# Optimization experiments

Measured on AMD Instinct MI355X. Metric: run time of the kernel, lower is better.

The kernel has to match this reference:

```python
import jax, jax.numpy as jnp
import numpy as np

G_K = 16
BN_EPS = 1e-5


def knn_idx(x, k):
    # x: (B, N, C) -> idx: (B, N, k) indices of k nearest neighbors (incl. self)
    sq = jnp.sum(x * x, axis=-1)                       # (B, N)
    d = sq[:, :, None] + sq[:, None, :] - 2.0 * jnp.einsum('bnc,bmc->bnm', x, x)
    _, idx = jax.lax.top_k(-d, k)                      # smallest distances
    return idx


def setup_inputs() -> dict:
    key = jax.random.key(0)
    k1, k2 = jax.random.split(key)
    B, N, C, D = 4, 8192, 3, 64
    x = jax.random.normal(k1, (B, N, C), dtype=jnp.float32)
    W = jax.random.normal(k2, (3 * C, D), dtype=jnp.float32) * 0.1
    b = jnp.zeros((D,), dtype=jnp.float32)
    gamma = jnp.ones((D,), dtype=jnp.float32)
    beta = jnp.zeros((D,), dtype=jnp.float32)
    return {"x": x, "W": W, "b": b, "gamma": gamma, "beta": beta}


def reference(x, W, b, gamma, beta):
    # KNN query (int indices, non-differentiable as in torch)
    idx = knn_idx(x, G_K)                              # (B, N, k)
    # gather-group neighbors: (B, N, k, C)
    x_ne = jax.vmap(lambda xb, ib: xb[ib])(x, idx)
    x_ce = jnp.broadcast_to(x[:, :, None, :], x_ne.shape)
    feat = jnp.concatenate([x_ce, x_ne - x_ce, x_ne], axis=-1)  # (B, N, k, 3C)
    # 1x1 conv == per-(point,neighbor) linear
    h = jnp.einsum('bnkc,cd->bnkd', feat, W) + b       # (B, N, k, D)
    # BatchNorm over (B, N, k) per channel (training-mode batch stats)
    mean = jnp.mean(h, axis=(0, 1, 2))
    var = jnp.var(h, axis=(0, 1, 2))
    h = gamma * (h - mean) * jax.lax.rsqrt(var + BN_EPS) + beta
    h = jax.nn.relu(h)
    # max-pool over neighbors k
    return jnp.max(h, axis=2)                          # (B, N, D)
```

## Files before the change

kernel.cpp:

```cpp
#include <hip/hip_runtime.h>

#define NPTS 8192
#define NB 4
#define KNN 16
#define DCH 64
#define CAP 128
#define WR 8

#define WS_XQ 0
#define WS_IB 524288
#define WS_ST 1572864
#define WS_SS 1573376

__device__ __forceinline__ float distf(float4 a, float4 c) {
    float dot = __fmaf_rn(a.x, c.x, __fmaf_rn(a.y, c.y, a.z * c.z));
    return __fmaf_rn(-2.0f, dot, a.w + c.w);
}

__global__ __launch_bounds__(256) void k1_prep(const float* __restrict__ x, float4* __restrict__ xq) {
    int p = blockIdx.x * 256 + threadIdx.x;
    if (p >= NB * NPTS) return;
    float x0 = x[p * 3 + 0], x1 = x[p * 3 + 1], x2 = x[p * 3 + 2];
    float sq = __fmaf_rn(x0, x0, __fmaf_rn(x1, x1, x2 * x2));
    xq[p] = make_float4(x0, x1, x2, sq);
}

__global__ __launch_bounds__(256, 4) void k2_knn(const float4* __restrict__ xq,
                                                 unsigned short* __restrict__ ibuf) {
    __shared__ float2 buf[4][WR][CAP];
    __shared__ float vmin[4][WR][64];
    const int wave = threadIdx.x >> 6;
    const int lane = threadIdx.x & 63;
    const int b = blockIdx.x >> 8;
    const int blkrow = (blockIdx.x & 255) * (4 * WR);
    const float4* xb = xq + b * NPTS;
    const int rowbase = blkrow + wave * WR;

    float4 xi[WR];
#pragma unroll
    for (int r = 0; r < WR; ++r) xi[r] = xb[rowbase + r];

    float mn[WR];
#pragma unroll
    for (int r = 0; r < WR; ++r) mn[r] = 3.0e38f;

#pragma unroll 2
    for (int c0 = 0; c0 < NPTS; c0 += 64) {
        float4 cj = xb[c0 + lane];
#pragma unroll
        for (int r = 0; r < WR; ++r) mn[r] = fminf(mn[r], distf(xi[r], cj));
    }

#pragma unroll
    for (int r = 0; r < WR; ++r) vmin[wave][r][lane] = mn[r];
    __syncthreads();

    float tau[WR];
#pragma unroll
    for (int r = 0; r < WR; ++r) {
        float mine = mn[r];
        int rk = 0;
        const float4* vm4 = (const float4*)(&vmin[wave][r][0]);
#pragma unroll
        for (int q = 0; q < 16; ++q) {
            float4 vv = vm4[q];
            int j0 = q * 4;
            rk += (vv.x < mine || (vv.x == mine && (j0 + 0) < lane)) ? 1 : 0;
            rk += (vv.y < mine || (vv.y == mine && (j0 + 1) < lane)) ? 1 : 0;
            rk += (vv.z < mine || (vv.z == mine && (j0 + 2) < lane)) ? 1 : 0;
            rk += (vv.w < mine || (vv.w == mine && (j0 + 3) < lane)) ? 1 : 0;
        }
        float v = (rk < KNN) ? mine : -3.0e38f;
#pragma unroll
        for (int o = 32; o > 0; o >>= 1) v = fmaxf(v, __shfl_xor(v, o));
        tau[r] = v;
    }

    int cnt[WR];
#pragma unroll
    for (int r = 0; r < WR; ++r) cnt[r] = 0;

#pragma unroll 2
    for (int c0 = 0; c0 < NPTS; c0 += 64) {
        float4 cj = xb[c0 + lane];
        float fidx = (float)(c0 + lane);
#pragma unroll
        for (int r = 0; r < WR; ++r) {
            float d = distf(xi[r], cj);
            bool pass = (d <= tau[r]);
            unsigned long long m = __ballot(pass);
            if (m) {
                if (pass) {
                    int ofs = __builtin_amdgcn_mbcnt_hi((unsigned)(m >> 32),
                              __builtin_amdgcn_mbcnt_lo((unsigned)m, 0));
                    int pos = cnt[r] + ofs;
                    if (pos < CAP) buf[wave][r][pos] = make_float2(d, fidx);
                }
                cnt[r] += (int)__popcll(m);
            }
        }
    }

    __syncthreads();

#pragma unroll
    for (int rr = 0; rr < WR; ++rr) {
        int n = cnt[rr];
        n = (n < CAP) ? n : CAP;
        int l1 = lane + 64;
        bool v0 = (lane < n), v1 = (l1 < n);
        float2 e0 = buf[wave][rr][v0 ? lane : 0];
        float2 e1 = buf[wave][rr][v1 ? l1 : 0];
        int r0 = 0, r1 = 0;
        for (int j = 0; j < n; ++j) {
            float2 fj = buf[wave][rr][j];
            r0 += (fj.x < e0.x || (fj.x == e0.x && fj.y < e0.y)) ? 1 : 0;
            r1 += (fj.x < e1.x || (fj.x == e1.x && fj.y < e1.y)) ? 1 : 0;
        }
        size_t grow = (size_t)(b * NPTS + rowbase + rr) * KNN;
        if (v0 && r0 < KNN) ibuf[grow + r0] = (unsigned short)(int)e0.y;
        if (v1 && r1 < KNN) ibuf[grow + r1] = (unsigned short)(int)e1.y;
    }
}

__global__ __launch_bounds__(256) void k3_moments(const float4* __restrict__ xq,
                                                  const unsigned short* __restrict__ ibuf,
                                                  double* __restrict__ stats) {
    __shared__ float red[4][54];
    int p = blockIdx.x * 256 + threadIdx.x;
    int b = p >> 13;
    const float4* xb = xq + b * NPTS;
    const unsigned short* ib = ibuf + (size_t)p * KNN;
    float4 xi = xb[p & (NPTS - 1)];

    float acc[54];
#pragma unroll
    for (int i = 0; i < 54; ++i) acc[i] = 0.0f;

#pragma unroll
    for (int k = 0; k < KNN; ++k) {
        int j = ib[k];
        float4 cj = xb[j];
        float f[9] = {xi.x, xi.y, xi.z, cj.x - xi.x, cj.y - xi.y, cj.z - xi.z, cj.x, cj.y, cj.z};
        int t = 9;
#pragma unroll
        for (int a = 0; a < 9; ++a) {
            acc[a] += f[a];
#pragma unroll
            for (int c = a; c < 9; ++c) { acc[t] += f[a] * f[c]; ++t; }
        }
    }

#pragma unroll
    for (int i = 0; i < 54; ++i) {
        float v = acc[i];
        for (int o = 32; o > 0; o >>= 1) v += __shfl_down(v, o);
        acc[i] = v;
    }
    int lane = threadIdx.x & 63;
    int wv = threadIdx.x >> 6;
    if (lane == 0) {
#pragma unroll
        for (int i = 0; i < 54; ++i) red[wv][i] = acc[i];
    }
    __syncthreads();
    if (threadIdx.x < 54) {
        float s = red[0][threadIdx.x] + red[1][threadIdx.x] + red[2][threadIdx.x] + red[3][threadIdx.x];
        atomicAdd(&stats[threadIdx.x], (double)s);
    }
}

__global__ void k4_finalize(const double* __restrict__ stats, const float* __restrict__ W,
                            const float* __restrict__ bias, const float* __restrict__ gamma,
                            const float* __restrict__ beta, float* __restrict__ ss) {
    int d = threadIdx.x;
    if (d >= DCH) return;
    const double M = (double)NB * NPTS * KNN;
    double w[9];
    for (int c = 0; c < 9; ++c) w[c] = (double)W[c * DCH + d];
    double mf[9];
    for (int a = 0; a < 9; ++a) mf[a] = stats[a] / M;
    double q1 = 0.0;
    for (int a = 0; a < 9; ++a) q1 += mf[a] * w[a];
    double q2 = 0.0;
    int t = 0;
    for (int a = 0; a < 9; ++a) {
        for (int c = a; c < 9; ++c) {
            double pv = stats[9 + t] / M;
            double term = pv * w[a] * w[c];
            q2 += (a == c) ? term : 2.0 * term;
            ++t;
        }
    }
    double bd = (double)bias[d];
    double mean = q1 + bd;
    double ehh = q2 + 2.0 * bd * q1 + bd * bd;
    double var = ehh - mean * mean;
    double sc = (double)gamma[d] / sqrt(var + 1e-5);
    double sh = (double)beta[d] + sc * (bd - mean);
    ss[d] = (float)sc;
    ss[DCH + d] = (float)sh;
}

__global__ __launch_bounds__(256) void k5_out(const float4* __restrict__ xq,
                                              const unsigned short* __restrict__ ibuf,
                                              const float* __restrict__ W, const float* __restrict__ ss,
                                              float* __restrict__ out) {
    __shared__ float Ws[9 * DCH];
    __shared__ float scs[DCH], shs[DCH];
    for (int i = threadIdx.x; i < 9 * DCH; i += 256) Ws[i] = W[i];
    if (threadIdx.x < DCH) {
        scs[threadIdx.x] = ss[threadIdx.x];
        shs[threadIdx.x] = ss[DCH + threadIdx.x];
    }
    __syncthreads();

    int pt = blockIdx.x * 32 + (threadIdx.x >> 3);
    int oc = (threadIdx.x & 7) * 8;
    int b = pt >> 13;
    const float4* xb = xq + b * NPTS;
    float4 xi = xb[pt & (NPTS - 1)];

    float w[9][8];
#pragma unroll
    for (int c = 0; c < 9; ++c)
#pragma unroll
        for (int d = 0; d < 8; ++d) w[c][d] = Ws[c * DCH + oc + d];
    float sc[8], sh[8], y[8];
#pragma unroll
    for (int d = 0; d < 8; ++d) {
        sc[d] = scs[oc + d];
        sh[d] = shs[oc + d];
        y[d] = 0.0f;
    }

    const unsigned short* ib = ibuf + (size_t)pt * KNN;
#pragma unroll
    for (int k = 0; k < KNN; ++k) {
        int j = ib[k];
        float4 cj = xb[j];
        float f[9] = {xi.x, xi.y, xi.z, cj.x - xi.x, cj.y - xi.y, cj.z - xi.z, cj.x, cj.y, cj.z};
        float h[8];
#pragma unroll
        for (int d = 0; d < 8; ++d) h[d] = 0.0f;
#pragma unroll
        for (int c = 0; c < 9; ++c)
#pragma unroll
            for (int d = 0; d < 8; ++d) h[d] = __fmaf_rn(f[c], w[c][d], h[d]);
#pragma unroll
        for (int d = 0; d < 8; ++d) {
            float v = __fmaf_rn(sc[d], h[d], sh[d]);
            y[d] = fmaxf(y[d], fmaxf(v, 0.0f));
        }
    }
    float4* o4 = (float4*)(out + (size_t)pt * DCH + oc);
    o4[0] = make_float4(y[0], y[1], y[2], y[3]);
    o4[1] = make_float4(y[4], y[5], y[6], y[7]);
}

extern "C" void kernel_launch(void* const* d_in, const int* in_sizes, int n_in,
                              void* d_out, int out_size, void* d_ws, size_t ws_size,
                              hipStream_t stream) {
    const float* x = (const float*)d_in[0];
    const float* W = (const float*)d_in[1];
    const float* bias = (const float*)d_in[2];
    const float* gamma = (const float*)d_in[3];
    const float* beta = (const float*)d_in[4];
    float* out = (float*)d_out;
    char* ws = (char*)d_ws;

    float4* xq = (float4*)(ws + WS_XQ);
    unsigned short* ibuf = (unsigned short*)(ws + WS_IB);
    double* stats = (double*)(ws + WS_ST);
    float* ss = (float*)(ws + WS_SS);

    hipMemsetAsync(stats, 0, 54 * sizeof(double), stream);
    k1_prep<<<128, 256, 0, stream>>>(x, xq);
    k2_knn<<<1024, 256, 0, stream>>>(xq, ibuf);
    k3_moments<<<128, 256, 0, stream>>>(xq, ibuf, stats);
    k4_finalize<<<1, 64, 0, stream>>>(stats, W, bias, gamma, beta, ss);
    k5_out<<<1024, 256, 0, stream>>>(xq, ibuf, W, ss, out);
}
```

Before: 149.1 us.

## Replace brute-force KNN scan with uniform-grid spatial binning and cell-range candidate lists

Points are binned into a 32^3 uniform grid per batch using an atomic count, a prefix scan and a scatter into cell-sorted order. Each wave of 8 spatially adjacent queries first takes an upper bound on its 16th-nearest distance from 64 nearby sorted points. It then gathers only the grid cells within that radius into a shared candidate list and runs the existing min and threshold-compaction passes over those candidates instead of all 8192 points. This cuts distance work from quadratic to near-local, at the cost of three extra small kernels, atomics and indirect gathers. It falls back to a full scan when the candidate list overflows.

```diff
diff --git a/kernel.cpp b/kernel.cpp
--- a/kernel.cpp
+++ b/kernel.cpp
@@ -6,61 +6,124 @@
 #define DCH 64
 #define CAP 128
 #define WR 8
+#define G 32
+#define NC 32768
+#define MCAP 2048
+#define HCEL 0.3125f
 
 #define WS_XQ 0
-#define WS_IB 524288
-#define WS_ST 1572864
-#define WS_SS 1573376
-
-__device__ __forceinline__ float distf(float4 a, float4 c) {
-    float dot = __fmaf_rn(a.x, c.x, __fmaf_rn(a.y, c.y, a.z * c.z));
-    return __fmaf_rn(-2.0f, dot, a.w + c.w);
-}
-
-__global__ __launch_bounds__(256) void k1_prep(const float* __restrict__ x, float4* __restrict__ xq) {
+#define WS_XS 524288
+#define WS_OI 1048576
+#define WS_IB 1114112
+#define WS_CP 2162688
+#define WS_ST 2686976
+#define WS_SS 2687488
+
+__device__ __forceinline__ float vkey(float4 q, float4 c) {
+    return __fmaf_rn(q.x, c.x, __fmaf_rn(q.y, c.y, __fmaf_rn(q.z, c.z, c.w)));
+}
+
+__device__ __forceinline__ int cellof(float v) {
+    float t = (v + 5.0f) * 3.2f;
+    t = fminf(fmaxf(t, 0.0f), 31.0f);
+    return (int)t;
+}
+
+__global__ __launch_bounds__(256) void k1_prep(const float* __restrict__ x, float4* __restrict__ xq,
+                                               int* __restrict__ cellP) {
     int p = blockIdx.x * 256 + threadIdx.x;
     if (p >= NB * NPTS) return;
+    int b = p >> 13;
     float x0 = x[p * 3 + 0], x1 = x[p * 3 + 1], x2 = x[p * 3 + 2];
     float sq = __fmaf_rn(x0, x0, __fmaf_rn(x1, x1, x2 * x2));
     xq[p] = make_float4(x0, x1, x2, sq);
-}
-
-__global__ __launch_bounds__(256, 4) void k2_knn(const float4* __restrict__ xq,
+    int cid = (cellof(x2) * G + cellof(x1)) * G + cellof(x0);
+    atomicAdd(&cellP[b * NC + cid], 1);
+}
+
+__global__ __launch_bounds__(1024) void k0b_prefix(int* __restrict__ P) {
+    __shared__ int part[1024];
+    int t = threadIdx.x;
+    int* Pb = P + blockIdx.x * NC;
+    int loc[32];
+    int s = 0;
+    int base = t * 32;
+#pragma unroll
+    for (int i = 0; i < 32; ++i) { loc[i] = Pb[base + i]; s += loc[i]; }
+    part[t] = s;
+    __syncthreads();
+    for (int off = 1; off < 1024; off <<= 1) {
+        int v = part[t];
+        if (t >= off) v += part[t - off];
+        __syncthreads();
+        part[t] = v;
+        __syncthreads();
+    }
+    int run = (t == 0) ? 0 : part[t - 1];
+#pragma unroll
+    for (int i = 0; i < 32; ++i) { int c = loc[i]; Pb[base + i] = run; run += c; }
+}
+
+__global__ __launch_bounds__(256) void k0c_scatter(const float* __restrict__ x, int* __restrict__ cellP,
+                                                   float4* __restrict__ xss, unsigned short* __restrict__ oidx) {
+    int p = blockIdx.x * 256 + threadIdx.x;
+    if (p >= NB * NPTS) return;
+    int b = p >> 13, pl = p & (NPTS - 1);
+    float x0 = x[p * 3 + 0], x1 = x[p * 3 + 1], x2 = x[p * 3 + 2];
+    float sq = __fmaf_rn(x0, x0, __fmaf_rn(x1, x1, x2 * x2));
+    int cid = (cellof(x2) * G + cellof(x1)) * G + cellof(x0);
+    int pos = atomicAdd(&cellP[b * NC + cid], 1);
+    xss[b * NPTS + pos] = make_float4(-2.0f * x0, -2.0f * x1, -2.0f * x2, sq);
+    oidx[b * NPTS + pos] = (unsigned short)pl;
+}
+
+__global__ __launch_bounds__(256, 3) void k2_knn(const float4* __restrict__ xq,
+                                                 const float4* __restrict__ xss,
+                                                 const unsigned short* __restrict__ oidx,
+                                                 const int* __restrict__ cellP,
                                                  unsigned short* __restrict__ ibuf) {
     __shared__ float2 buf[4][WR][CAP];
-    __shared__ float vmin[4][WR][64];
+    __shared__ unsigned short sidx[4][MCAP];
     const int wave = threadIdx.x >> 6;
     const int lane = threadIdx.x & 63;
     const int b = blockIdx.x >> 8;
-    const int blkrow = (blockIdx.x & 255) * (4 * WR);
-    const float4* xb = xq + b * NPTS;
-    const int rowbase = blkrow + wave * WR;
+    const int js = (blockIdx.x & 255) * 32 + wave * WR;
+    const float4* xqb = xq + b * NPTS;
+    const float4* xsb = xss + b * NPTS;
+    const unsigned short* oib = oidx + b * NPTS;
+    const int* Pb = cellP + b * NC;
+    float* vw = (float*)&buf[wave][0][0];
 
     float4 xi[WR];
-#pragma unroll
-    for (int r = 0; r < WR; ++r) xi[r] = xb[rowbase + r];
-
-    float mn[WR];
-#pragma unroll
-    for (int r = 0; r < WR; ++r) mn[r] = 3.0e38f;
-
-#pragma unroll 2
-    for (int c0 = 0; c0 < NPTS; c0 += 64) {
-        float4 cj = xb[c0 + lane];
-#pragma unroll
-        for (int r = 0; r < WR; ++r) mn[r] = fminf(mn[r], distf(xi[r], cj));
-    }
-
-#pragma unroll
-    for (int r = 0; r < WR; ++r) vmin[wave][r][lane] = mn[r];
-    __syncthreads();
-
-    float tau[WR];
+    int orow[WR];
 #pragma unroll
     for (int r = 0; r < WR; ++r) {
-        float mine = mn[r];
+        int o = oib[js + r];
+        orow[r] = o;
+        xi[r] = xqb[o];
+    }
+
+    float bxl = xi[0].x, bxh = xi[0].x, byl = xi[0].y, byh = xi[0].y, bzl = xi[0].z, bzh = xi[0].z;
+#pragma unroll
+    for (int r = 1; r < WR; ++r) {
+        bxl = fminf(bxl, xi[r].x); bxh = fmaxf(bxh, xi[r].x);
+        byl = fminf(byl, xi[r].y); byh = fmaxf(byh, xi[r].y);
+        bzl = fminf(bzl, xi[r].z); bzh = fmaxf(bzh, xi[r].z);
+    }
+
+    int w0 = js - 28;
+    w0 = w0 < 0 ? 0 : (w0 > NPTS - 64 ? NPTS - 64 : w0);
+    float4 cw = xsb[w0 + lane];
+    float v0s[WR];
+#pragma unroll
+    for (int r = 0; r < WR; ++r) { v0s[r] = vkey(xi[r], cw); vw[r * 64 + lane] = v0s[r]; }
+    __syncthreads();
+    float taudmax = 0.0f;
+#pragma unroll
+    for (int r = 0; r < WR; ++r) {
+        float mine = v0s[r];
         int rk = 0;
-        const float4* vm4 = (const float4*)(&vmin[wave][r][0]);
+        const float4* vm4 = (const float4*)(vw + r * 64);
 #pragma unroll
         for (int q = 0; q < 16; ++q) {
             float4 vv = vm4[q];
@@ -73,28 +136,100 @@
         float v = (rk < KNN) ? mine : -3.0e38f;
 #pragma unroll
         for (int o = 32; o > 0; o >>= 1) v = fmaxf(v, __shfl_xor(v, o));
+        taudmax = fmaxf(taudmax, v + xi[r].w);
+    }
+    taudmax = fmaxf(taudmax, 0.0f);
+    float rmax = sqrtf(taudmax);
+
+    int cx0 = cellof(bxl - rmax), cx1 = cellof(bxh + rmax);
+    int cy0 = cellof(byl - rmax), cy1 = cellof(byh + rmax);
+    int cz0 = cellof(bzl - rmax), cz1 = cellof(bzh + rmax);
+
+    int M = 0;
+    for (int iz = cz0; iz <= cz1; ++iz) {
+        float zl = (iz == 0) ? -1.0e30f : (-5.0f + iz * HCEL);
+        float zh = (iz == G - 1) ? 1.0e30f : (-5.0f + (iz + 1) * HCEL);
+        float dz = fmaxf(0.0f, fmaxf(zl - bzh, bzl - zh));
+        float dz2 = dz * dz;
+        if (dz2 > taudmax) continue;
+        for (int iy = cy0; iy <= cy1; ++iy) {
+            float yl = (iy == 0) ? -1.0e30f : (-5.0f + iy * HCEL);
+            float yh = (iy == G - 1) ? 1.0e30f : (-5.0f + (iy + 1) * HCEL);
+            float dy = fmaxf(0.0f, fmaxf(yl - byh, byl - yh));
+            float dd = __fmaf_rn(dy, dy, dz2);
+            if (dd > taudmax) continue;
+            int cb = (iz * G + iy) * G;
+            int cs = cb + cx0, ce = cb + cx1;
+            int s0 = (cs == 0) ? 0 : Pb[cs - 1];
+            int e0 = Pb[ce];
+            for (int q0 = s0; q0 < e0; q0 += 64) {
+                int len = e0 - q0; len = len < 64 ? len : 64;
+                int pos = M + lane;
+                if (lane < len && pos < MCAP) sidx[wave][pos] = (unsigned short)(q0 + lane);
+                M += len;
+            }
+        }
+    }
+    __syncthreads();
+    const bool fb = (M > MCAP);
+    const int Ms = fb ? NPTS : M;
+
+    float mn[WR];
+#pragma unroll
+    for (int r = 0; r < WR; ++r) mn[r] = 3.0e38f;
+    for (int q0 = 0; q0 < Ms; q0 += 64) {
+        int t_ = q0 + lane;
+        bool act = t_ < Ms;
+        int idx = fb ? t_ : (int)sidx[wave][act ? t_ : 0];
+        float4 c = act ? xsb[idx] : make_float4(0.0f, 0.0f, 0.0f, 3.0e38f);
+#pragma unroll
+        for (int r = 0; r < WR; ++r) mn[r] = fminf(mn[r], vkey(xi[r], c));
+    }
+
+#pragma unroll
+    for (int r = 0; r < WR; ++r) vw[r * 64 + lane] = mn[r];
+    __syncthreads();
+    float tau[WR];
+#pragma unroll
+    for (int r = 0; r < WR; ++r) {
+        float mine = mn[r];
+        int rk = 0;
+        const float4* vm4 = (const float4*)(vw + r * 64);
+#pragma unroll
+        for (int q = 0; q < 16; ++q) {
+            float4 vv = vm4[q];
+            int j0 = q * 4;
+            rk += (vv.x < mine || (vv.x == mine && (j0 + 0) < lane)) ? 1 : 0;
+            rk += (vv.y < mine || (vv.y == mine && (j0 + 1) < lane)) ? 1 : 0;
+            rk += (vv.z < mine || (vv.z == mine && (j0 + 2) < lane)) ? 1 : 0;
+            rk += (vv.w < mine || (vv.w == mine && (j0 + 3) < lane)) ? 1 : 0;
+        }
+        float v = (rk < KNN) ? mine : -3.0e38f;
+#pragma unroll
+        for (int o = 32; o > 0; o >>= 1) v = fmaxf(v, __shfl_xor(v, o));
         tau[r] = v;
     }
 
     int cnt[WR];
 #pragma unroll
     for (int r = 0; r < WR; ++r) cnt[r] = 0;
-
-#pragma unroll 2
-    for (int c0 = 0; c0 < NPTS; c0 += 64) {
-        float4 cj = xb[c0 + lane];
-        float fidx = (float)(c0 + lane);
+    for (int q0 = 0; q0 < Ms; q0 += 64) {
+        int t_ = q0 + lane;
+        bool act = t_ < Ms;
+        int idx = fb ? t_ : (int)sidx[wave][act ? t_ : 0];
+        float4 c = act ? xsb[idx] : make_float4(0.0f, 0.0f, 0.0f, 3.0e38f);
+        float fo = act ? (float)oib[idx] : 0.0f;
 #pragma unroll
         for (int r = 0; r < WR; ++r) {
-            float d = distf(xi[r], cj);
-            bool pass = (d <= tau[r]);
-            unsigned long long m = __ballot(pass);
+            float v = vkey(xi[r], c);
+            bool p = (v <= tau[r]);
+            unsigned long long m = __ballot(p);
             if (m) {
-                if (pass) {
+                if (p) {
                     int ofs = __builtin_amdgcn_mbcnt_hi((unsigned)(m >> 32),
                               __builtin_amdgcn_mbcnt_lo((unsigned)m, 0));
                     int pos = cnt[r] + ofs;
-                    if (pos < CAP) buf[wave][r][pos] = make_float2(d, fidx);
+                    if (pos < CAP) buf[wave][r][pos] = make_float2(v, fo);
                 }
                 cnt[r] += (int)__popcll(m);
             }
@@ -117,7 +252,7 @@
             r0 += (fj.x < e0.x || (fj.x == e0.x && fj.y < e0.y)) ? 1 : 0;
             r1 += (fj.x < e1.x || (fj.x == e1.x && fj.y < e1.y)) ? 1 : 0;
         }
-        size_t grow = (size_t)(b * NPTS + rowbase + rr) * KNN;
+        size_t grow = (size_t)(b * NPTS + orow[rr]) * KNN;
         if (v0 && r0 < KNN) ibuf[grow + r0] = (unsigned short)(int)e0.y;
         if (v1 && r1 < KNN) ibuf[grow + r1] = (unsigned short)(int)e1.y;
     }
@@ -270,13 +405,19 @@
     char* ws = (char*)d_ws;
 
     float4* xq = (float4*)(ws + WS_XQ);
+    float4* xss = (float4*)(ws + WS_XS);
+    unsigned short* oidx = (unsigned short*)(ws + WS_OI);
     unsigned short* ibuf = (unsigned short*)(ws + WS_IB);
+    int* cellP = (int*)(ws + WS_CP);
     double* stats = (double*)(ws + WS_ST);
     float* ss = (float*)(ws + WS_SS);
 
+    hipMemsetAsync(cellP, 0, NB * NC * sizeof(int), stream);
     hipMemsetAsync(stats, 0, 54 * sizeof(double), stream);
-    k1_prep<<<128, 256, 0, stream>>>(x, xq);
-    k2_knn<<<1024, 256, 0, stream>>>(xq, ibuf);
+    k1_prep<<<128, 256, 0, stream>>>(x, xq, cellP);
+    k0b_prefix<<<NB, 1024, 0, stream>>>(cellP);
+    k0c_scatter<<<128, 256, 0, stream>>>(x, cellP, xss, oidx);
+    k2_knn<<<1024, 256, 0, stream>>>(xq, xss, oidx, cellP, ibuf);
     k3_moments<<<128, 256, 0, stream>>>(xq, ibuf, stats);
     k4_finalize<<<1, 64, 0, stream>>>(stats, W, bias, gamma, beta, ss);
     k5_out<<<1024, 256, 0, stream>>>(xq, ibuf, W, ss, out);
```

Result: slower. 483.4 us (+224.2%).

## Bin points by x-coordinate to restrict KNN candidate scans to a slab

Applied to the files above, without the earlier changes.

Adds a counting-sort pass that bins points by x into 256 bins and scatters them into sorted order along with their original indices. The KNN kernel first gets an approximate 16th-neighbour radius from a 1024-point window of sorted neighbours, then scans only the x-slab of bins that radius can reach, for both the refined threshold and the candidate collection. This replaces the full O(N) scan per row with a much narrower range. In exchange it adds three small kernels, atomics and extra workspace, and hard-codes bin bounds of [-5,5] tuned to Gaussian inputs (clamping keeps results correct outside that range).

```diff
diff --git a/kernel.cpp b/kernel.cpp
--- a/kernel.cpp
+++ b/kernel.cpp
@@ -6,61 +6,120 @@
 #define DCH 64
 #define CAP 128
 #define WR 8
+#define NBIN 256
 
 #define WS_XQ 0
-#define WS_IB 524288
-#define WS_ST 1572864
-#define WS_SS 1573376
-
-__device__ __forceinline__ float distf(float4 a, float4 c) {
-    float dot = __fmaf_rn(a.x, c.x, __fmaf_rn(a.y, c.y, a.z * c.z));
-    return __fmaf_rn(-2.0f, dot, a.w + c.w);
-}
-
-__global__ __launch_bounds__(256) void k1_prep(const float* __restrict__ x, float4* __restrict__ xq) {
+#define WS_QS 524288
+#define WS_XS 1048576
+#define WS_OI 1572864
+#define WS_IB 1638400
+#define WS_P  2686976
+#define WS_ST 2691072
+#define WS_SS 2691584
+
+__device__ __forceinline__ float vkey(float4 q, float4 c) {
+    return __fmaf_rn(q.x, c.x, __fmaf_rn(q.y, c.y, __fmaf_rn(q.z, c.z, c.w)));
+}
+
+__device__ __forceinline__ int binof(float v) {
+    float t = (v + 5.0f) * 25.6f;
+    t = fminf(fmaxf(t, 0.0f), 255.0f);
+    return (int)t;
+}
+
+__global__ __launch_bounds__(256) void k1_prep(const float* __restrict__ x, float4* __restrict__ xq,
+                                               int* __restrict__ P) {
     int p = blockIdx.x * 256 + threadIdx.x;
     if (p >= NB * NPTS) return;
+    int b = p >> 13;
     float x0 = x[p * 3 + 0], x1 = x[p * 3 + 1], x2 = x[p * 3 + 2];
     float sq = __fmaf_rn(x0, x0, __fmaf_rn(x1, x1, x2 * x2));
     xq[p] = make_float4(x0, x1, x2, sq);
-}
-
-__global__ __launch_bounds__(256, 4) void k2_knn(const float4* __restrict__ xq,
+    atomicAdd(&P[b * NBIN + binof(x0)], 1);
+}
+
+__global__ __launch_bounds__(256) void k0b_prefix(int* __restrict__ P) {
+    __shared__ int s[NBIN];
+    int t = threadIdx.x;
+    int* Pb = P + blockIdx.x * NBIN;
+    s[t] = Pb[t];
+    __syncthreads();
+    for (int o = 1; o < NBIN; o <<= 1) {
+        int u = (t >= o) ? s[t - o] : 0;
+        __syncthreads();
+        s[t] += u;
+        __syncthreads();
+    }
+    Pb[t] = (t == 0) ? 0 : s[t - 1];
+}
+
+__global__ __launch_bounds__(256) void k0c_scatter(const float* __restrict__ x, int* __restrict__ P,
+                                                   float4* __restrict__ xqs, float4* __restrict__ xss,
+                                                   unsigned short* __restrict__ oidx) {
+    int p = blockIdx.x * 256 + threadIdx.x;
+    if (p >= NB * NPTS) return;
+    int b = p >> 13, pl = p & (NPTS - 1);
+    float x0 = x[p * 3 + 0], x1 = x[p * 3 + 1], x2 = x[p * 3 + 2];
+    float sq = __fmaf_rn(x0, x0, __fmaf_rn(x1, x1, x2 * x2));
+    int pos = atomicAdd(&P[b * NBIN + binof(x0)], 1);
+    xqs[b * NPTS + pos] = make_float4(x0, x1, x2, sq);
+    xss[b * NPTS + pos] = make_float4(-2.0f * x0, -2.0f * x1, -2.0f * x2, sq);
+    oidx[b * NPTS + pos] = (unsigned short)pl;
+}
+
+__global__ __launch_bounds__(256, 4) void k2_knn(const float4* __restrict__ xqs,
+                                                 const float4* __restrict__ xss,
+                                                 const unsigned short* __restrict__ oidx,
+                                                 const int* __restrict__ P,
                                                  unsigned short* __restrict__ ibuf) {
     __shared__ float2 buf[4][WR][CAP];
-    __shared__ float vmin[4][WR][64];
+    __shared__ int preL[NBIN + 1];
     const int wave = threadIdx.x >> 6;
     const int lane = threadIdx.x & 63;
     const int b = blockIdx.x >> 8;
-    const int blkrow = (blockIdx.x & 255) * (4 * WR);
-    const float4* xb = xq + b * NPTS;
-    const int rowbase = blkrow + wave * WR;
+    const int js = (blockIdx.x & 255) * 32 + wave * WR;
+    const float4* xqb = xqs + b * NPTS;
+    const float4* xsb = xss + b * NPTS;
+    const unsigned short* oib = oidx + b * NPTS;
+    float* vw = (float*)&buf[wave][0][0];
+
+    if (threadIdx.x < NBIN) preL[threadIdx.x + 1] = P[b * NBIN + threadIdx.x];
+    if (threadIdx.x == 0) preL[0] = 0;
 
     float4 xi[WR];
-#pragma unroll
-    for (int r = 0; r < WR; ++r) xi[r] = xb[rowbase + r];
+    int orow[WR];
+#pragma unroll
+    for (int r = 0; r < WR; ++r) {
+        int sp = js + r;
+        xi[r] = xqb[sp];
+        orow[r] = oib[sp];
+    }
+    __syncthreads();
 
     float mn[WR];
 #pragma unroll
     for (int r = 0; r < WR; ++r) mn[r] = 3.0e38f;
-
-#pragma unroll 2
-    for (int c0 = 0; c0 < NPTS; c0 += 64) {
-        float4 cj = xb[c0 + lane];
-#pragma unroll
-        for (int r = 0; r < WR; ++r) mn[r] = fminf(mn[r], distf(xi[r], cj));
-    }
-
-#pragma unroll
-    for (int r = 0; r < WR; ++r) vmin[wave][r][lane] = mn[r];
-    __syncthreads();
-
-    float tau[WR];
+    {
+        int w0 = js + 4 - 512;
+        w0 = w0 < 0 ? 0 : (w0 > NPTS - 1024 ? NPTS - 1024 : w0);
+        const float4* pp = xsb + w0 + lane;
+#pragma unroll 4
+        for (int k = 0; k < 16; ++k) {
+            float4 c = pp[k * 64];
+#pragma unroll
+            for (int r = 0; r < WR; ++r) mn[r] = fminf(mn[r], vkey(xi[r], c));
+        }
+    }
+#pragma unroll
+    for (int r = 0; r < WR; ++r) vw[r * 64 + lane] = mn[r];
+    __syncthreads();
+
+    int lo = NPTS, hi = 0;
 #pragma unroll
     for (int r = 0; r < WR; ++r) {
         float mine = mn[r];
         int rk = 0;
-        const float4* vm4 = (const float4*)(&vmin[wave][r][0]);
+        const float4* vm4 = (const float4*)(vw + r * 64);
 #pragma unroll
         for (int q = 0; q < 16; ++q) {
             float4 vv = vm4[q];
@@ -73,28 +132,67 @@
         float v = (rk < KNN) ? mine : -3.0e38f;
 #pragma unroll
         for (int o = 32; o > 0; o >>= 1) v = fmaxf(v, __shfl_xor(v, o));
+        float taud = fmaxf(v + xi[r].w, 0.0f);
+        float r0 = sqrtf(taud) * 1.0001f + 1.0e-6f;
+        int blo = binof(xi[r].x - r0);
+        int bhi = binof(xi[r].x + r0);
+        int l_ = preL[blo], h_ = preL[bhi + 1];
+        lo = l_ < lo ? l_ : lo;
+        hi = h_ > hi ? h_ : hi;
+    }
+
+#pragma unroll
+    for (int r = 0; r < WR; ++r) mn[r] = 3.0e38f;
+    for (int t0 = lo; t0 < hi; t0 += 64) {
+        int t = t0 + lane;
+        float4 c = (t < hi) ? xsb[t] : make_float4(0.0f, 0.0f, 0.0f, 3.0e38f);
+#pragma unroll
+        for (int r = 0; r < WR; ++r) mn[r] = fminf(mn[r], vkey(xi[r], c));
+    }
+
+#pragma unroll
+    for (int r = 0; r < WR; ++r) vw[r * 64 + lane] = mn[r];
+    __syncthreads();
+    float tau[WR];
+#pragma unroll
+    for (int r = 0; r < WR; ++r) {
+        float mine = mn[r];
+        int rk = 0;
+        const float4* vm4 = (const float4*)(vw + r * 64);
+#pragma unroll
+        for (int q = 0; q < 16; ++q) {
+            float4 vv = vm4[q];
+            int j0 = q * 4;
+            rk += (vv.x < mine || (vv.x == mine && (j0 + 0) < lane)) ? 1 : 0;
+            rk += (vv.y < mine || (vv.y == mine && (j0 + 1) < lane)) ? 1 : 0;
+            rk += (vv.z < mine || (vv.z == mine && (j0 + 2) < lane)) ? 1 : 0;
+            rk += (vv.w < mine || (vv.w == mine && (j0 + 3) < lane)) ? 1 : 0;
+        }
+        float v = (rk < KNN) ? mine : -3.0e38f;
+#pragma unroll
+        for (int o = 32; o > 0; o >>= 1) v = fmaxf(v, __shfl_xor(v, o));
         tau[r] = v;
     }
 
     int cnt[WR];
 #pragma unroll
     for (int r = 0; r < WR; ++r) cnt[r] = 0;
-
-#pragma unroll 2
-    for (int c0 = 0; c0 < NPTS; c0 += 64) {
-        float4 cj = xb[c0 + lane];
-        float fidx = (float)(c0 + lane);
+    for (int t0 = lo; t0 < hi; t0 += 64) {
+        int t = t0 + lane;
+        bool act = t < hi;
+        float4 c = act ? xsb[t] : make_float4(0.0f, 0.0f, 0.0f, 3.0e38f);
+        float fo = act ? (float)oib[t] : 0.0f;
 #pragma unroll
         for (int r = 0; r < WR; ++r) {
-            float d = distf(xi[r], cj);
-            bool pass = (d <= tau[r]);
-            unsigned long long m = __ballot(pass);
+            float v = vkey(xi[r], c);
+            bool pp = (v <= tau[r]);
+            unsigned long long m = __ballot(pp);
             if (m) {
-                if (pass) {
+                if (pp) {
                     int ofs = __builtin_amdgcn_mbcnt_hi((unsigned)(m >> 32),
                               __builtin_amdgcn_mbcnt_lo((unsigned)m, 0));
                     int pos = cnt[r] + ofs;
-                    if (pos < CAP) buf[wave][r][pos] = make_float2(d, fidx);
+                    if (pos < CAP) buf[wave][r][pos] = make_float2(v, fo);
                 }
                 cnt[r] += (int)__popcll(m);
             }
@@ -117,7 +215,7 @@
             r0 += (fj.x < e0.x || (fj.x == e0.x && fj.y < e0.y)) ? 1 : 0;
             r1 += (fj.x < e1.x || (fj.x == e1.x && fj.y < e1.y)) ? 1 : 0;
         }
-        size_t grow = (size_t)(b * NPTS + rowbase + rr) * KNN;
+        size_t grow = (size_t)(b * NPTS + orow[rr]) * KNN;
         if (v0 && r0 < KNN) ibuf[grow + r0] = (unsigned short)(int)e0.y;
         if (v1 && r1 < KNN) ibuf[grow + r1] = (unsigned short)(int)e1.y;
     }
@@ -270,13 +368,20 @@
     char* ws = (char*)d_ws;
 
     float4* xq = (float4*)(ws + WS_XQ);
+    float4* xqs = (float4*)(ws + WS_QS);
+    float4* xss = (float4*)(ws + WS_XS);
+    unsigned short* oidx = (unsigned short*)(ws + WS_OI);
     unsigned short* ibuf = (unsigned short*)(ws + WS_IB);
+    int* P = (int*)(ws + WS_P);
     double* stats = (double*)(ws + WS_ST);
     float* ss = (float*)(ws + WS_SS);
 
+    hipMemsetAsync(P, 0, NB * NBIN * sizeof(int), stream);
     hipMemsetAsync(stats, 0, 54 * sizeof(double), stream);
-    k1_prep<<<128, 256, 0, stream>>>(x, xq);
-    k2_knn<<<1024, 256, 0, stream>>>(xq, ibuf);
+    k1_prep<<<128, 256, 0, stream>>>(x, xq, P);
+    k0b_prefix<<<NB, 256, 0, stream>>>(P);
+    k0c_scatter<<<128, 256, 0, stream>>>(x, P, xqs, xss, oidx);
+    k2_knn<<<1024, 256, 0, stream>>>(xqs, xss, oidx, P, ibuf);
     k3_moments<<<128, 256, 0, stream>>>(xq, ibuf, stats);
     k4_finalize<<<1, 64, 0, stream>>>(stats, W, bias, gamma, beta, ss);
     k5_out<<<1024, 256, 0, stream>>>(xq, ibuf, W, ss, out);
```

Result: slower. 196.7 us (+31.9%).
